# Performance work log

Hardware: AMD Instinct MI355X
Metric: run time of the kernel (lower is better)

## Reference

```python
import jax, jax.numpy as jnp
import numpy as np

H = 16          # n_heads
HID = 64        # QASS MLP hidden dim


def setup_inputs() -> dict:
    key = jax.random.key(0)
    ks = jax.random.split(key, 12)
    B, N, D = 2, 2048, 1024
    Dh = D // H
    inp = {
        "query": jax.random.normal(ks[0], (B, N, D), jnp.float32),
        "key": jax.random.normal(ks[1], (B, N, D), jnp.float32),
        "value": jax.random.normal(ks[2], (B, N, D), jnp.float32),
        "allowed_mask": jnp.ones((1, 1, N, N), dtype=bool),
        # projection weights, torch Linear convention: y = x @ W.T, W: [out, in]
        "wq": jax.random.normal(ks[3], (D, D), jnp.float32) * (D ** -0.5),
        "wk": jax.random.normal(ks[4], (D, D), jnp.float32) * (D ** -0.5),
        "wv": jax.random.normal(ks[5], (D, D), jnp.float32) * (D ** -0.5),
        "wo": jax.random.normal(ks[6], (D, D), jnp.float32) * (D ** -0.5),
        # QASS scaler weights
        "wb1": jax.random.normal(ks[7], (HID, 1), jnp.float32),          # mlp_base[0]
        "wb2": jax.random.normal(ks[8], (H * Dh, HID), jnp.float32) * (HID ** -0.5),  # mlp_base[2]
        "wg1": jax.random.normal(ks[9], (HID, Dh), jnp.float32) * (Dh ** -0.5),       # mlp_gate[0]
        "wg2": jax.random.normal(ks[10], (Dh, HID), jnp.float32) * (HID ** -0.5),     # mlp_gate[2]
        "n_context": 2048,
    }
    return inp


def _gelu(x):
    return jax.nn.gelu(x, approximate=False)  # torch nn.GELU default (erf)


def reference(query, key, value, allowed_mask, wq, wk, wv, wo, wb1, wb2, wg1, wg2, n_context):
    B, N, D = query.shape
    Dh = D // H

    def split_heads(x):  # [B,N,D] -> [B,H,N,Dh]
        return x.reshape(B, N, H, Dh).transpose(0, 2, 1, 3)

    q = split_heads(query @ wq.T)
    k = split_heads(key @ wk.T)
    v = split_heads(value @ wv.T)

    # QASS scaling: q * base(log n) * (1 + tanh(gate(q)))   (n_context > 1)
    log_n = jnp.log(jnp.asarray(n_context, jnp.float32))
    base = (_gelu(log_n * wb1[:, 0]) @ wb2.T).reshape(1, H, 1, Dh)  # [1,H,1,Dh]
    gate = 1.0 + jnp.tanh(_gelu(q @ wg1.T) @ wg2.T)                  # [B,H,N,Dh]
    q = q * base * gate

    scores = jnp.einsum("bhnd,bhmd->bhnm", q, k) / jnp.sqrt(jnp.float32(Dh))
    scores = jnp.where(allowed_mask, scores, -jnp.inf)
    attn = jax.nn.softmax(scores, axis=-1)  # dropout p=0 -> identity
    out = jnp.einsum("bhnm,bhmd->bhnd", attn, v)
    out = out.transpose(0, 2, 1, 3).reshape(B, N, D)
    return out @ wo.T
```

## Files before the change

### kernel.cpp

```cpp
#include <hip/hip_runtime.h>
#include <math.h>


typedef _Float16 half_t;
using half8   = __attribute__((ext_vector_type(8))) _Float16;
using bhalf8  = __attribute__((ext_vector_type(8))) short;
using floatx4 = __attribute__((ext_vector_type(4))) float;

__device__ inline unsigned short f2bf(float f) {
  union { float f; unsigned int u; } v; v.f = f;
  unsigned int u = v.u;
  u = u + 0x7fffu + ((u >> 16) & 1u);
  return (unsigned short)(u >> 16);
}
__device__ inline float bf2f(unsigned short h) {
  union { unsigned int u; float f; } v; v.u = ((unsigned int)h) << 16;
  return v.f;
}
__device__ inline float gelu_f(float x) {
  return 0.5f * x * (1.0f + erff(x * 0.70710678118654752440f));
}

#define MFMAF16(a, b, c)  __builtin_amdgcn_mfma_f32_16x16x32_f16((a), (b), (c), 0, 0, 0)
#define MFMABF16(a, b, c) __builtin_amdgcn_mfma_f32_16x16x32_bf16((a), (b), (c), 0, 0, 0)

__device__ __forceinline__ void dma16(const void* g, void* l) {
  __builtin_amdgcn_global_load_lds(
      (const __attribute__((address_space(1))) unsigned int*)g,
      (__attribute__((address_space(3))) unsigned int*)l, 16, 0, 0);
}

__global__ __launch_bounds__(256) void k_cvtbase(
    const float* __restrict__ q, const float* __restrict__ k, const float* __restrict__ v,
    const float* __restrict__ wq, const float* __restrict__ wk,
    const float* __restrict__ wv, const float* __restrict__ wo,
    half_t* __restrict__ q16, half_t* __restrict__ k16, half_t* __restrict__ v16,
    half_t* __restrict__ w16,
    const float* __restrict__ wb1, const float* __restrict__ wb2,
    const int* __restrict__ nctx, float* __restrict__ base_out) {
  int tid = threadIdx.x;
  if (blockIdx.x >= 8192) {
    __shared__ float h1[64];
    float logn = logf((float)(*nctx));
    if (tid < 64) h1[tid] = gelu_f(logn * wb1[tid]);
    __syncthreads();
    int i = (blockIdx.x - 8192) * 256 + tid;
    float s = 0.f;
#pragma unroll
    for (int j = 0; j < 64; j++) s += h1[j] * wb2[i * 64 + j];
    base_out[i] = s;
    return;
  }
  size_t e = ((size_t)blockIdx.x * 256 + tid) * 8;
  const float* src; half_t* dst; size_t off;
  if (e < (size_t)3 * 4194304) {
    int t = (int)(e >> 22); off = e & 4194303;
    src = (t == 0) ? q : (t == 1 ? k : v);
    dst = (t == 0) ? q16 : (t == 1 ? k16 : v16);
  } else {
    size_t e2 = e - (size_t)3 * 4194304;
    int t = (int)(e2 >> 20); off = (e2 & 1048575);
    src = (t == 0) ? wq : (t == 1 ? wk : (t == 2 ? wv : wo));
    dst = w16 + (size_t)t * 1048576;
  }
  float4 a = *(const float4*)(src + off);
  float4 b = *(const float4*)(src + off + 4);
  half8 h;
  h[0] = (half_t)a.x; h[1] = (half_t)a.y; h[2] = (half_t)a.z; h[3] = (half_t)a.w;
  h[4] = (half_t)b.x; h[5] = (half_t)b.y; h[6] = (half_t)b.z; h[7] = (half_t)b.w;
  *(half8*)(dst + off) = h;
}

template <int MODE>
__global__ __launch_bounds__(256, 3) void k_gemm(const half_t* __restrict__ Abase,
                                                 const half_t* __restrict__ Wbase,
                                                 half_t* __restrict__ qp16,
                                                 half_t* __restrict__ kswz,
                                                 unsigned short* __restrict__ vtl,
                                                 float* __restrict__ outf) {
  const int z = (MODE == 0) ? blockIdx.z : 0;
  const half_t* Ag = Abase + (size_t)z * 4194304;
  const half_t* Wg = Wbase + (size_t)z * 1048576;
  __shared__ __align__(16) half_t As[128 * 64];
  __shared__ __align__(16) half_t Bs[128 * 64];
  const int tid = threadIdx.x, lane = tid & 63, w = tid >> 6;
  const int quad = lane >> 4, lm = lane & 15, a7 = lm & 7;
  const int wm = w >> 1, wn = w & 1;
  const int bm0 = blockIdx.y * 128, bn0 = blockIdx.x * 128;

  const floatx4 zero4 = {0.f, 0.f, 0.f, 0.f};
  floatx4 acc[4][4];
#pragma unroll
  for (int i = 0; i < 4; i++)
#pragma unroll
    for (int j = 0; j < 4; j++) acc[i][j] = zero4;

  for (int kk = 0; kk < 1024; kk += 64) {
    __syncthreads();
#pragma unroll
    for (int i = 0; i < 4; i++) {
      int tr = w * 32 + i * 8 + (lane >> 3);
      int c = (lane & 7) ^ (tr & 7);
      dma16((const char*)Ag + ((size_t)(bm0 + tr) * 1024 + kk + c * 8) * 2,
            (char*)As + (w * 32 + i * 8) * 128);
      dma16((const char*)Wg + ((size_t)(bn0 + tr) * 1024 + kk + c * 8) * 2,
            (char*)Bs + (w * 32 + i * 8) * 128);
    }
    __syncthreads();

#pragma unroll
    for (int kc = 0; kc < 2; kc++) {
      half8 af[4], bf[4];
#pragma unroll
      for (int tm = 0; tm < 4; tm++)
        af[tm] = *(const half8*)&As[(wm * 64 + tm * 16 + lm) * 64
                                    + (((kc * 4 + quad) ^ a7) << 3)];
#pragma unroll
      for (int tn = 0; tn < 4; tn++)
        bf[tn] = *(const half8*)&Bs[(wn * 64 + tn * 16 + lm) * 64
                                    + (((kc * 4 + quad) ^ a7) << 3)];
#pragma unroll
      for (int tm = 0; tm < 4; tm++)
#pragma unroll
        for (int tn = 0; tn < 4; tn++)
          acc[tm][tn] = MFMAF16(af[tm], bf[tn], acc[tm][tn]);
    }
  }

#pragma unroll
  for (int tm = 0; tm < 4; tm++)
#pragma unroll
    for (int tn = 0; tn < 4; tn++)
#pragma unroll
      for (int rr = 0; rr < 4; rr++) {
        int gm = bm0 + wm * 64 + tm * 16 + quad * 4 + rr;
        int gn = bn0 + wn * 64 + tn * 16 + lm;
        float v = acc[tm][tn][rr];
        if constexpr (MODE == 3) {
          outf[(size_t)gm * 1024 + gn] = v;
        } else {
          int b = gm >> 11, n = gm & 2047, hd = gn >> 6, d = gn & 63;
          if (z == 0) {
            qp16[((size_t)((b << 4) + hd) * 2048 + n) * 64 + d] = (half_t)v;
          } else if (z == 1) {
            size_t rowb = ((size_t)((b << 4) + hd) * 2048 + n) * 64;
            kswz[rowb + (size_t)((((d >> 3) ^ (n & 7)) << 3) | (d & 7))] = (half_t)v;
          } else {
            int t = n >> 6, nn = n & 63;
            int pos = ((nn & 15) << 2) | ((nn >> 4) & 3);
            size_t idx = ((size_t)(((b << 4) + hd) * 32 + t) * 64 + d) * 64
                       + (size_t)((((pos >> 3) ^ (d & 7)) * 8) + (pos & 7));
            vtl[idx] = f2bf(v);
          }
        }
      }
}

__global__ __launch_bounds__(256) void k_gate(const half_t* __restrict__ qp,
                                              const float* __restrict__ base_v,
                                              const float* __restrict__ wg1,
                                              const float* __restrict__ wg2,
                                              half_t* __restrict__ qs) {
  __shared__ __align__(16) half_t W1[64 * 72];
  __shared__ __align__(16) half_t W2[64 * 72];
  __shared__ __align__(16) half_t HT[4][16 * 72];
  const int tid = threadIdx.x, lane = tid & 63, w = tid >> 6;
  const int quad = lane >> 4, lm = lane & 15;
  for (int i = tid; i < 4096; i += 256) {
    int j = i >> 6, d = i & 63;
    W1[j * 72 + d] = (half_t)wg1[i];
    W2[j * 72 + d] = (half_t)wg2[i];
  }
  __syncthreads();
  const int R0 = blockIdx.x * 256;
  const int hd = (R0 >> 11) & 15;
  float bsev[4];
#pragma unroll
  for (int tn = 0; tn < 4; tn++) bsev[tn] = base_v[hd * 64 + tn * 16 + lm];
  const float cs = 0.18033688011112042f;
  const floatx4 zero4 = {0.f, 0.f, 0.f, 0.f};
  half_t* ht = HT[w];

  for (int ti = 0; ti < 4; ti++) {
    int r0 = R0 + w * 64 + ti * 16;
    half8 aq0 = *(const half8*)&qp[(size_t)(r0 + lm) * 64 + quad * 8];
    half8 aq1 = *(const half8*)&qp[(size_t)(r0 + lm) * 64 + 32 + quad * 8];
    floatx4 hc[4];
#pragma unroll
    for (int tn = 0; tn < 4; tn++) {
      half8 b0 = *(const half8*)&W1[(tn * 16 + lm) * 72 + quad * 8];
      half8 b1 = *(const half8*)&W1[(tn * 16 + lm) * 72 + 32 + quad * 8];
      floatx4 t = zero4;
      t = MFMAF16(aq0, b0, t);
      t = MFMAF16(aq1, b1, t);
      hc[tn] = t;
    }
#pragma unroll
    for (int tn = 0; tn < 4; tn++)
#pragma unroll
      for (int rr = 0; rr < 4; rr++)
        ht[(quad * 4 + rr) * 72 + tn * 16 + lm] = (half_t)gelu_f(hc[tn][rr]);
    half8 ah0 = *(const half8*)&ht[lm * 72 + quad * 8];
    half8 ah1 = *(const half8*)&ht[lm * 72 + 32 + quad * 8];
#pragma unroll
    for (int tn = 0; tn < 4; tn++) {
      half8 b0 = *(const half8*)&W2[(tn * 16 + lm) * 72 + quad * 8];
      half8 b1 = *(const half8*)&W2[(tn * 16 + lm) * 72 + 32 + quad * 8];
      floatx4 t = zero4;
      t = MFMAF16(ah0, b0, t);
      t = MFMAF16(ah1, b1, t);
#pragma unroll
      for (int rr = 0; rr < 4; rr++) {
        int row = r0 + quad * 4 + rr;
        int d = tn * 16 + lm;
        float qv = (float)qp[(size_t)row * 64 + d];
        float g = 1.0f + tanhf(t[rr]);
        qs[(size_t)row * 64 + d] = (half_t)(qv * bsev[tn] * g * cs);
      }
    }
  }
}

__global__ __launch_bounds__(256, 2) void k_attn(const half_t* __restrict__ qs,
                                                 const half_t* __restrict__ kswz,
                                                 const unsigned short* __restrict__ vtl,
                                                 unsigned short* __restrict__ Opart,
                                                 float* __restrict__ rpart) {
  __shared__ __align__(16) half_t KH[2][64 * 64];
  __shared__ __align__(16) unsigned short VT[2][64 * 64];
  constexpr int PS = 68;
  __shared__ __align__(16) unsigned short PL[4][16 * PS];

  const int tid = threadIdx.x;
  const int lane = tid & 63;
  const int w = tid >> 6;
  const int quad = lane >> 4;
  const int lm = lane & 15;
  const int a7 = lm & 7;
  const int hd = blockIdx.x;
  const int qg = blockIdx.y >> 1, half = blockIdx.y & 1;
  const int b = blockIdx.z;
  const int bh = b * 16 + hd;
  const size_t hb = (size_t)bh * 2048 * 64;
  const char* khT = (const char*)(kswz + hb);
  const char* vtT = (const char*)(vtl + (size_t)bh * 32 * 4096);

  half8 qh[4][2];
#pragma unroll
  for (int rg = 0; rg < 4; rg++)
#pragma unroll
    for (int kc = 0; kc < 2; kc++)
      qh[rg][kc] = *(const half8*)(qs + hb
          + (size_t)(qg * 256 + w * 64 + rg * 16 + lm) * 64 + kc * 32 + quad * 8);

  const floatx4 zero4 = {0.f, 0.f, 0.f, 0.f};
  floatx4 O[4][4];
#pragma unroll
  for (int rg = 0; rg < 4; rg++)
#pragma unroll
    for (int dt = 0; dt < 4; dt++) O[rg][dt] = zero4;
  float rsum[4][4];
#pragma unroll
  for (int rg = 0; rg < 4; rg++)
#pragma unroll
    for (int rr = 0; rr < 4; rr++) rsum[rg][rr] = 0.f;

  unsigned short* plw = PL[w];
  const int lo16 = lane * 16;
  const size_t g0 = (size_t)half * 16 * 8192;

#pragma unroll
  for (int r = 0; r < 2; r++) {
    int sb = (w * 2 + r) * 1024;
    dma16(khT + g0 + sb + lo16, (char*)KH[0] + sb);
    dma16(vtT + g0 + sb + lo16, (char*)VT[0] + sb);
  }

  for (int t = 0; t < 16; t++) {
    const int cur = t & 1;
    __syncthreads();
    if (t < 15) {
      const int nb = cur ^ 1;
      const size_t gof = g0 + (size_t)(t + 1) * 8192;
#pragma unroll
      for (int r = 0; r < 2; r++) {
        int sb = (w * 2 + r) * 1024;
        dma16(khT + gof + sb + lo16, (char*)KH[nb] + sb);
        dma16(vtT + gof + sb + lo16, (char*)VT[nb] + sb);
      }
    }

    const half_t* kh_ = KH[cur];
    const unsigned short* vt_ = VT[cur];

    bhalf8 vf[2][4];
#pragma unroll
    for (int kc4 = 0; kc4 < 2; kc4++)
#pragma unroll
      for (int dt = 0; dt < 4; dt++)
        vf[kc4][dt] = *(const bhalf8*)
            &vt_[(dt * 16 + lm) * 64 + (((kc4 * 4 + quad) ^ a7) << 3)];

#pragma unroll
    for (int p = 0; p < 2; p++) {
      floatx4 s[2][4];
#pragma unroll
      for (int ri = 0; ri < 2; ri++)
#pragma unroll
        for (int kb = 0; kb < 4; kb++) s[ri][kb] = zero4;

      __builtin_amdgcn_s_setprio(1);
#pragma unroll
      for (int kb = 0; kb < 4; kb++)
#pragma unroll
        for (int kc = 0; kc < 2; kc++) {
          int addr = (kb * 16 + lm) * 64 + (((kc * 4 + quad) ^ a7) << 3);
          half8 khf = *(const half8*)&kh_[addr];
#pragma unroll
          for (int ri = 0; ri < 2; ri++)
            s[ri][kb] = MFMAF16(qh[p * 2 + ri][kc], khf, s[ri][kb]);
        }
      __builtin_amdgcn_s_setprio(0);

#pragma unroll
      for (int ri = 0; ri < 2; ri++) {
        const int rg = p * 2 + ri;
#pragma unroll
        for (int rr = 0; rr < 4; rr++) {
          float p0 = __builtin_amdgcn_exp2f(s[ri][0][rr]);
          float p1 = __builtin_amdgcn_exp2f(s[ri][1][rr]);
          float p2 = __builtin_amdgcn_exp2f(s[ri][2][rr]);
          float p3 = __builtin_amdgcn_exp2f(s[ri][3][rr]);
          rsum[rg][rr] += (p0 + p1) + (p2 + p3);
          unsigned int u0 = __float_as_uint(p0) + 0x8000u;
          unsigned int u1 = __float_as_uint(p1) + 0x8000u;
          unsigned int u2 = __float_as_uint(p2) + 0x8000u;
          unsigned int u3 = __float_as_uint(p3) + 0x8000u;
          uint2 pk;
          pk.x = __builtin_amdgcn_perm(u1, u0, 0x07060302u);
          pk.y = __builtin_amdgcn_perm(u3, u2, 0x07060302u);
          *(uint2*)&plw[(quad * 4 + rr) * PS + lm * 4] = pk;
        }
        __builtin_amdgcn_s_setprio(1);
#pragma unroll
        for (int kc4 = 0; kc4 < 2; kc4++) {
          bhalf8 pf = *(const bhalf8*)&plw[lm * PS + kc4 * 32 + quad * 8];
#pragma unroll
          for (int dt = 0; dt < 4; dt++)
            O[rg][dt] = MFMABF16(pf, vf[kc4][dt], O[rg][dt]);
        }
        __builtin_amdgcn_s_setprio(0);
      }
    }
  }

  unsigned short* op = Opart + (size_t)half * 65536 * 64;
  float* rp = rpart + (size_t)half * 65536;
#pragma unroll
  for (int rg = 0; rg < 4; rg++)
#pragma unroll
    for (int rr = 0; rr < 4; rr++) {
      float rs = rsum[rg][rr];
      rs += __shfl_xor(rs, 1, 64);
      rs += __shfl_xor(rs, 2, 64);
      rs += __shfl_xor(rs, 4, 64);
      rs += __shfl_xor(rs, 8, 64);
      int n = qg * 256 + w * 64 + rg * 16 + quad * 4 + rr;
      size_t row = (size_t)bh * 2048 + n;
      if (lm == 0) rp[row] = rs;
#pragma unroll
      for (int dt = 0; dt < 4; dt++)
        op[row * 64 + dt * 16 + lm] = f2bf(O[rg][dt][rr]);
    }
}

__global__ __launch_bounds__(256) void k_combine(const unsigned short* __restrict__ Opart,
                                                 const float* __restrict__ rpart,
                                                 half_t* __restrict__ obf) {
  size_t e = ((size_t)blockIdx.x * 256 + threadIdx.x) * 8;
  size_t row = e >> 6; int d0 = (int)(e & 63);
  float inv = 1.0f / (rpart[row] + rpart[65536 + row]);
  bhalf8 o0 = *(const bhalf8*)&Opart[row * 64 + d0];
  bhalf8 o1 = *(const bhalf8*)&Opart[(size_t)65536 * 64 + row * 64 + d0];
  int b = (int)(row >> 15), h = (int)((row >> 11) & 15), n = (int)(row & 2047);
  half8 o;
#pragma unroll
  for (int j = 0; j < 8; j++)
    o[j] = (half_t)((bf2f((unsigned short)o0[j]) + bf2f((unsigned short)o1[j])) * inv);
  *(half8*)&obf[((size_t)(b * 2048 + n)) * 1024 + h * 64 + d0] = o;
}

extern "C" void kernel_launch(void* const* d_in, const int* in_sizes, int n_in,
                              void* d_out, int out_size, void* d_ws, size_t ws_size,
                              hipStream_t stream) {
  const float* query = (const float*)d_in[0];
  const float* key_  = (const float*)d_in[1];
  const float* value = (const float*)d_in[2];
  const float* wq  = (const float*)d_in[4];
  const float* wk  = (const float*)d_in[5];
  const float* wv  = (const float*)d_in[6];
  const float* wo  = (const float*)d_in[7];
  const float* wb1 = (const float*)d_in[8];
  const float* wb2 = (const float*)d_in[9];
  const float* wg1 = (const float*)d_in[10];
  const float* wg2 = (const float*)d_in[11];
  const int* nctx  = (const int*)d_in[12];
  float* out = (float*)d_out;

  char* ws = (char*)d_ws;
  size_t o = 0;
  float* base_v = (float*)(ws + o); o += 4096;
  half_t* q16   = (half_t*)(ws + o); o += (size_t)4096 * 1024 * 2;
  half_t* k16   = (half_t*)(ws + o); o += (size_t)4096 * 1024 * 2;
  half_t* v16   = (half_t*)(ws + o); o += (size_t)4096 * 1024 * 2;
  half_t* w16   = (half_t*)(ws + o); o += (size_t)4 * 1024 * 1024 * 2;
  half_t* qp16  = (half_t*)(ws + o); o += (size_t)4096 * 1024 * 2;
  half_t* kswz  = (half_t*)(ws + o); o += (size_t)4096 * 1024 * 2;
  unsigned short* vtl = (unsigned short*)(ws + o); o += (size_t)4096 * 1024 * 2;
  unsigned short* Opart = (unsigned short*)(ws + o); o += (size_t)2 * 65536 * 64 * 2;
  float* rpart = (float*)(ws + o); o += (size_t)2 * 65536 * 4;
  half_t* qs  = q16;
  half_t* obf = k16;

  k_cvtbase<<<8196, 256, 0, stream>>>(query, key_, value, wq, wk, wv, wo,
                                      q16, k16, v16, w16, wb1, wb2, nctx, base_v);
  k_gemm<0><<<dim3(8, 32, 3), 256, 0, stream>>>(q16, w16, qp16, kswz, vtl, nullptr);
  k_gate<<<256, 256, 0, stream>>>(qp16, base_v, wg1, wg2, qs);
  k_attn<<<dim3(16, 16, 2), 256, 0, stream>>>(qs, kswz, vtl, Opart, rpart);
  k_combine<<<2048, 256, 0, stream>>>(Opart, rpart, obf);
  k_gemm<3><<<dim3(8, 32, 1), 256, 0, stream>>>(obf, w16 + (size_t)3 * 1048576,
                                                nullptr, nullptr, nullptr, out);
}
```

Baseline: 276.9 us.

## Split attention KV into four chunks and load V fragments directly from global

The attention grid now splits the 2048-key sequence into four chunks of 512 instead of two. This doubles the block count to improve occupancy across compute units, and the combine kernel now sums four partial outputs and row sums. The V projection epilogue writes V in a per-lane MFMA fragment order, so each wave reads its V operands straight from global memory into registers. That removes the V shared-memory buffer and its DMA staging. The trade-offs are more partial-output traffic and combine work, un-prefetched global V loads in the inner loop, and a workspace re-layout that aliases the larger partial buffer over the no-longer-needed v16/qp16 regions.

```diff
diff --git a/kernel.cpp b/kernel.cpp
--- a/kernel.cpp
+++ b/kernel.cpp
@@ -147,9 +147,11 @@
             kswz[rowb + (size_t)((((d >> 3) ^ (n & 7)) << 3) | (d & 7))] = (half_t)v;
           } else {
             int t = n >> 6, nn = n & 63;
-            int pos = ((nn & 15) << 2) | ((nn >> 4) & 3);
-            size_t idx = ((size_t)(((b << 4) + hd) * 32 + t) * 64 + d) * 64
-                       + (size_t)((((pos >> 3) ^ (d & 7)) * 8) + (pos & 7));
+            int kc4 = (nn >> 3) & 1;
+            int qd  = (nn >> 1) & 3;
+            int jj  = ((nn & 1) << 2) | (nn >> 4);
+            size_t idx = ((size_t)(((b << 4) + hd) * 32 + t) * 2 + kc4) * 2048
+                       + (size_t)((qd * 16 + (d & 15)) * 32 + (d >> 4) * 8 + jj);
             vtl[idx] = f2bf(v);
           }
         }
@@ -227,7 +229,6 @@
                                                  unsigned short* __restrict__ Opart,
                                                  float* __restrict__ rpart) {
   __shared__ __align__(16) half_t KH[2][64 * 64];
-  __shared__ __align__(16) unsigned short VT[2][64 * 64];
   constexpr int PS = 68;
   __shared__ __align__(16) unsigned short PL[4][16 * PS];
 
@@ -238,12 +239,12 @@
   const int lm = lane & 15;
   const int a7 = lm & 7;
   const int hd = blockIdx.x;
-  const int qg = blockIdx.y >> 1, half = blockIdx.y & 1;
+  const int qg = blockIdx.y >> 2, ks = blockIdx.y & 3;
   const int b = blockIdx.z;
   const int bh = b * 16 + hd;
   const size_t hb = (size_t)bh * 2048 * 64;
   const char* khT = (const char*)(kswz + hb);
-  const char* vtT = (const char*)(vtl + (size_t)bh * 32 * 4096);
+  const unsigned short* vtT = vtl + (size_t)bh * 32 * 4096;
 
   half8 qh[4][2];
 #pragma unroll
@@ -267,39 +268,36 @@
 
   unsigned short* plw = PL[w];
   const int lo16 = lane * 16;
-  const size_t g0 = (size_t)half * 16 * 8192;
+  const size_t g0 = (size_t)ks * 65536;
 
 #pragma unroll
   for (int r = 0; r < 2; r++) {
     int sb = (w * 2 + r) * 1024;
     dma16(khT + g0 + sb + lo16, (char*)KH[0] + sb);
-    dma16(vtT + g0 + sb + lo16, (char*)VT[0] + sb);
-  }
-
-  for (int t = 0; t < 16; t++) {
+  }
+
+  for (int t = 0; t < 8; t++) {
     const int cur = t & 1;
     __syncthreads();
-    if (t < 15) {
-      const int nb = cur ^ 1;
+
+    const unsigned short* vb = vtT + ((size_t)(ks * 8 + t) * 2) * 2048 + lane * 32;
+    bhalf8 vf[2][4];
+#pragma unroll
+    for (int kc4 = 0; kc4 < 2; kc4++)
+#pragma unroll
+      for (int dt = 0; dt < 4; dt++)
+        vf[kc4][dt] = *(const bhalf8*)(vb + kc4 * 2048 + dt * 8);
+
+    if (t < 7) {
       const size_t gof = g0 + (size_t)(t + 1) * 8192;
 #pragma unroll
       for (int r = 0; r < 2; r++) {
         int sb = (w * 2 + r) * 1024;
-        dma16(khT + gof + sb + lo16, (char*)KH[nb] + sb);
-        dma16(vtT + gof + sb + lo16, (char*)VT[nb] + sb);
+        dma16(khT + gof + sb + lo16, (char*)KH[cur ^ 1] + sb);
       }
     }
 
     const half_t* kh_ = KH[cur];
-    const unsigned short* vt_ = VT[cur];
-
-    bhalf8 vf[2][4];
-#pragma unroll
-    for (int kc4 = 0; kc4 < 2; kc4++)
-#pragma unroll
-      for (int dt = 0; dt < 4; dt++)
-        vf[kc4][dt] = *(const bhalf8*)
-            &vt_[(dt * 16 + lm) * 64 + (((kc4 * 4 + quad) ^ a7) << 3)];
 
 #pragma unroll
     for (int p = 0; p < 2; p++) {
@@ -354,8 +352,8 @@
     }
   }
 
-  unsigned short* op = Opart + (size_t)half * 65536 * 64;
-  float* rp = rpart + (size_t)half * 65536;
+  unsigned short* op = Opart + (size_t)ks * 65536 * 64;
+  float* rp = rpart + (size_t)ks * 65536;
 #pragma unroll
   for (int rg = 0; rg < 4; rg++)
 #pragma unroll
@@ -379,14 +377,18 @@
                                                  half_t* __restrict__ obf) {
   size_t e = ((size_t)blockIdx.x * 256 + threadIdx.x) * 8;
   size_t row = e >> 6; int d0 = (int)(e & 63);
-  float inv = 1.0f / (rpart[row] + rpart[65536 + row]);
+  float inv = 1.0f / (rpart[row] + rpart[65536 + row]
+                    + rpart[131072 + row] + rpart[196608 + row]);
   bhalf8 o0 = *(const bhalf8*)&Opart[row * 64 + d0];
-  bhalf8 o1 = *(const bhalf8*)&Opart[(size_t)65536 * 64 + row * 64 + d0];
+  bhalf8 o1 = *(const bhalf8*)&Opart[(size_t)1 * 65536 * 64 + row * 64 + d0];
+  bhalf8 o2 = *(const bhalf8*)&Opart[(size_t)2 * 65536 * 64 + row * 64 + d0];
+  bhalf8 o3 = *(const bhalf8*)&Opart[(size_t)3 * 65536 * 64 + row * 64 + d0];
   int b = (int)(row >> 15), h = (int)((row >> 11) & 15), n = (int)(row & 2047);
   half8 o;
 #pragma unroll
   for (int j = 0; j < 8; j++)
-    o[j] = (half_t)((bf2f((unsigned short)o0[j]) + bf2f((unsigned short)o1[j])) * inv);
+    o[j] = (half_t)(((bf2f((unsigned short)o0[j]) + bf2f((unsigned short)o1[j]))
+                   + (bf2f((unsigned short)o2[j]) + bf2f((unsigned short)o3[j]))) * inv);
   *(half8*)&obf[((size_t)(b * 2048 + n)) * 1024 + h * 64 + d0] = o;
 }
 
@@ -413,12 +415,14 @@
   half_t* q16   = (half_t*)(ws + o); o += (size_t)4096 * 1024 * 2;
   half_t* k16   = (half_t*)(ws + o); o += (size_t)4096 * 1024 * 2;
   half_t* v16   = (half_t*)(ws + o); o += (size_t)4096 * 1024 * 2;
+  half_t* qp16  = (half_t*)(ws + o); o += (size_t)4096 * 1024 * 2;
+  unsigned short* OpartC = (unsigned short*)(ws + o); o += (size_t)2 * 65536 * 64 * 2;
+  float* rpart = (float*)(ws + o); o += (size_t)4 * 65536 * 4;
   half_t* w16   = (half_t*)(ws + o); o += (size_t)4 * 1024 * 1024 * 2;
-  half_t* qp16  = (half_t*)(ws + o); o += (size_t)4096 * 1024 * 2;
   half_t* kswz  = (half_t*)(ws + o); o += (size_t)4096 * 1024 * 2;
   unsigned short* vtl = (unsigned short*)(ws + o); o += (size_t)4096 * 1024 * 2;
-  unsigned short* Opart = (unsigned short*)(ws + o); o += (size_t)2 * 65536 * 64 * 2;
-  float* rpart = (float*)(ws + o); o += (size_t)2 * 65536 * 4;
+  (void)OpartC;
+  unsigned short* Opart = (unsigned short*)v16;
   half_t* qs  = q16;
   half_t* obf = k16;
 
@@ -426,7 +430,7 @@
                                       q16, k16, v16, w16, wb1, wb2, nctx, base_v);
   k_gemm<0><<<dim3(8, 32, 3), 256, 0, stream>>>(q16, w16, qp16, kswz, vtl, nullptr);
   k_gate<<<256, 256, 0, stream>>>(qp16, base_v, wg1, wg2, qs);
-  k_attn<<<dim3(16, 16, 2), 256, 0, stream>>>(qs, kswz, vtl, Opart, rpart);
+  k_attn<<<dim3(16, 32, 2), 256, 0, stream>>>(qs, kswz, vtl, Opart, rpart);
   k_combine<<<2048, 256, 0, stream>>>(Opart, rpart, obf);
   k_gemm<3><<<dim3(8, 32, 1), 256, 0, stream>>>(obf, w16 + (size_t)3 * 1048576,
                                                 nullptr, nullptr, nullptr, out);
```

After: 298.7 us. +7.9%, slower.

## Compute transposed scores to keep P in registers and load V directly

Applied to the files above, without the earlier changes.

The attention kernel now computes S^T by swapping the MFMA operands, so each lane holds the scores for one query row across keys. That lets the bf16 P fragment be packed in registers for the PV MFMA, with no round trip through LDS, and the row sums reduce with two shuffles instead of four. The V projection now writes a new lane-ordered global layout so V fragments are read straight from global memory instead of being DMA'd into LDS. This removes LDS traffic and shared memory use, but adds uncovered global-load latency for V at the start of each tile.

```diff
diff --git a/kernel.cpp b/kernel.cpp
--- a/kernel.cpp
+++ b/kernel.cpp
@@ -147,9 +147,11 @@
             kswz[rowb + (size_t)((((d >> 3) ^ (n & 7)) << 3) | (d & 7))] = (half_t)v;
           } else {
             int t = n >> 6, nn = n & 63;
-            int pos = ((nn & 15) << 2) | ((nn >> 4) & 3);
-            size_t idx = ((size_t)(((b << 4) + hd) * 32 + t) * 64 + d) * 64
-                       + (size_t)((((pos >> 3) ^ (d & 7)) * 8) + (pos & 7));
+            int kc4 = nn >> 5;
+            int qd  = (nn >> 2) & 3;
+            int jj  = (nn & 3) | (((nn >> 4) & 1) << 2);
+            size_t idx = ((size_t)(((b << 4) + hd) * 32 + t) * 2 + kc4) * 2048
+                       + (size_t)((qd * 16 + (d & 15)) * 32 + (d >> 4) * 8 + jj);
             vtl[idx] = f2bf(v);
           }
         }
@@ -227,9 +229,6 @@
                                                  unsigned short* __restrict__ Opart,
                                                  float* __restrict__ rpart) {
   __shared__ __align__(16) half_t KH[2][64 * 64];
-  __shared__ __align__(16) unsigned short VT[2][64 * 64];
-  constexpr int PS = 68;
-  __shared__ __align__(16) unsigned short PL[4][16 * PS];
 
   const int tid = threadIdx.x;
   const int lane = tid & 63;
@@ -243,7 +242,7 @@
   const int bh = b * 16 + hd;
   const size_t hb = (size_t)bh * 2048 * 64;
   const char* khT = (const char*)(kswz + hb);
-  const char* vtT = (const char*)(vtl + (size_t)bh * 32 * 4096);
+  const unsigned short* vtT = vtl + (size_t)bh * 32 * 4096;
 
   half8 qh[4][2];
 #pragma unroll
@@ -259,13 +258,8 @@
   for (int rg = 0; rg < 4; rg++)
 #pragma unroll
     for (int dt = 0; dt < 4; dt++) O[rg][dt] = zero4;
-  float rsum[4][4];
-#pragma unroll
-  for (int rg = 0; rg < 4; rg++)
-#pragma unroll
-    for (int rr = 0; rr < 4; rr++) rsum[rg][rr] = 0.f;
-
-  unsigned short* plw = PL[w];
+  float rsum[4] = {0.f, 0.f, 0.f, 0.f};
+
   const int lo16 = lane * 16;
   const size_t g0 = (size_t)half * 16 * 8192;
 
@@ -273,33 +267,30 @@
   for (int r = 0; r < 2; r++) {
     int sb = (w * 2 + r) * 1024;
     dma16(khT + g0 + sb + lo16, (char*)KH[0] + sb);
-    dma16(vtT + g0 + sb + lo16, (char*)VT[0] + sb);
   }
 
   for (int t = 0; t < 16; t++) {
     const int cur = t & 1;
     __syncthreads();
+
+    const unsigned short* vb = vtT + ((size_t)(half * 16 + t) * 2) * 2048 + lane * 32;
+    bhalf8 vf[2][4];
+#pragma unroll
+    for (int kc4 = 0; kc4 < 2; kc4++)
+#pragma unroll
+      for (int dt = 0; dt < 4; dt++)
+        vf[kc4][dt] = *(const bhalf8*)(vb + kc4 * 2048 + dt * 8);
+
     if (t < 15) {
-      const int nb = cur ^ 1;
       const size_t gof = g0 + (size_t)(t + 1) * 8192;
 #pragma unroll
       for (int r = 0; r < 2; r++) {
         int sb = (w * 2 + r) * 1024;
-        dma16(khT + gof + sb + lo16, (char*)KH[nb] + sb);
-        dma16(vtT + gof + sb + lo16, (char*)VT[nb] + sb);
+        dma16(khT + gof + sb + lo16, (char*)KH[cur ^ 1] + sb);
       }
     }
 
     const half_t* kh_ = KH[cur];
-    const unsigned short* vt_ = VT[cur];
-
-    bhalf8 vf[2][4];
-#pragma unroll
-    for (int kc4 = 0; kc4 < 2; kc4++)
-#pragma unroll
-      for (int dt = 0; dt < 4; dt++)
-        vf[kc4][dt] = *(const bhalf8*)
-            &vt_[(dt * 16 + lm) * 64 + (((kc4 * 4 + quad) ^ a7) << 3)];
 
 #pragma unroll
     for (int p = 0; p < 2; p++) {
@@ -318,36 +309,41 @@
           half8 khf = *(const half8*)&kh_[addr];
 #pragma unroll
           for (int ri = 0; ri < 2; ri++)
-            s[ri][kb] = MFMAF16(qh[p * 2 + ri][kc], khf, s[ri][kb]);
+            s[ri][kb] = MFMAF16(khf, qh[p * 2 + ri][kc], s[ri][kb]);
         }
       __builtin_amdgcn_s_setprio(0);
 
 #pragma unroll
       for (int ri = 0; ri < 2; ri++) {
         const int rg = p * 2 + ri;
-#pragma unroll
-        for (int rr = 0; rr < 4; rr++) {
-          float p0 = __builtin_amdgcn_exp2f(s[ri][0][rr]);
-          float p1 = __builtin_amdgcn_exp2f(s[ri][1][rr]);
-          float p2 = __builtin_amdgcn_exp2f(s[ri][2][rr]);
-          float p3 = __builtin_amdgcn_exp2f(s[ri][3][rr]);
-          rsum[rg][rr] += (p0 + p1) + (p2 + p3);
-          unsigned int u0 = __float_as_uint(p0) + 0x8000u;
-          unsigned int u1 = __float_as_uint(p1) + 0x8000u;
-          unsigned int u2 = __float_as_uint(p2) + 0x8000u;
-          unsigned int u3 = __float_as_uint(p3) + 0x8000u;
-          uint2 pk;
-          pk.x = __builtin_amdgcn_perm(u1, u0, 0x07060302u);
-          pk.y = __builtin_amdgcn_perm(u3, u2, 0x07060302u);
-          *(uint2*)&plw[(quad * 4 + rr) * PS + lm * 4] = pk;
-        }
+        float e[4][4];
+#pragma unroll
+        for (int kb = 0; kb < 4; kb++)
+#pragma unroll
+          for (int rr = 0; rr < 4; rr++)
+            e[kb][rr] = __builtin_amdgcn_exp2f(s[ri][kb][rr]);
+        rsum[rg] += (((e[0][0] + e[0][1]) + (e[0][2] + e[0][3]))
+                   + ((e[1][0] + e[1][1]) + (e[1][2] + e[1][3])))
+                  + (((e[2][0] + e[2][1]) + (e[2][2] + e[2][3]))
+                   + ((e[3][0] + e[3][1]) + (e[3][2] + e[3][3])));
+        unsigned int u[4][4];
+#pragma unroll
+        for (int kb = 0; kb < 4; kb++)
+#pragma unroll
+          for (int rr = 0; rr < 4; rr++)
+            u[kb][rr] = __float_as_uint(e[kb][rr]) + 0x8000u;
+
         __builtin_amdgcn_s_setprio(1);
 #pragma unroll
         for (int kc4 = 0; kc4 < 2; kc4++) {
-          bhalf8 pf = *(const bhalf8*)&plw[lm * PS + kc4 * 32 + quad * 8];
+          union { unsigned int w4[4]; bhalf8 v; } pa;
+          pa.w4[0] = __builtin_amdgcn_perm(u[2 * kc4][1], u[2 * kc4][0], 0x07060302u);
+          pa.w4[1] = __builtin_amdgcn_perm(u[2 * kc4][3], u[2 * kc4][2], 0x07060302u);
+          pa.w4[2] = __builtin_amdgcn_perm(u[2 * kc4 + 1][1], u[2 * kc4 + 1][0], 0x07060302u);
+          pa.w4[3] = __builtin_amdgcn_perm(u[2 * kc4 + 1][3], u[2 * kc4 + 1][2], 0x07060302u);
 #pragma unroll
           for (int dt = 0; dt < 4; dt++)
-            O[rg][dt] = MFMABF16(pf, vf[kc4][dt], O[rg][dt]);
+            O[rg][dt] = MFMABF16(pa.v, vf[kc4][dt], O[rg][dt]);
         }
         __builtin_amdgcn_s_setprio(0);
       }
@@ -357,21 +353,21 @@
   unsigned short* op = Opart + (size_t)half * 65536 * 64;
   float* rp = rpart + (size_t)half * 65536;
 #pragma unroll
-  for (int rg = 0; rg < 4; rg++)
+  for (int rg = 0; rg < 4; rg++) {
+    float rs = rsum[rg];
+    rs += __shfl_xor(rs, 16, 64);
+    rs += __shfl_xor(rs, 32, 64);
+    if (lane < 16)
+      rp[(size_t)bh * 2048 + qg * 256 + w * 64 + rg * 16 + lm] = rs;
 #pragma unroll
     for (int rr = 0; rr < 4; rr++) {
-      float rs = rsum[rg][rr];
-      rs += __shfl_xor(rs, 1, 64);
-      rs += __shfl_xor(rs, 2, 64);
-      rs += __shfl_xor(rs, 4, 64);
-      rs += __shfl_xor(rs, 8, 64);
       int n = qg * 256 + w * 64 + rg * 16 + quad * 4 + rr;
       size_t row = (size_t)bh * 2048 + n;
-      if (lm == 0) rp[row] = rs;
 #pragma unroll
       for (int dt = 0; dt < 4; dt++)
         op[row * 64 + dt * 16 + lm] = f2bf(O[rg][dt][rr]);
     }
+  }
 }
 
 __global__ __launch_bounds__(256) void k_combine(const unsigned short* __restrict__ Opart,
```

Result: slower. 291.2 us (+5.2%).
